# Kernel optimization log

Hardware: AMD Instinct MI355X
Metric: run time of the kernel (lower is better)

The kernel has to match this reference:

```python
import jax, jax.numpy as jnp
import numpy as np

B = 16384
F_IN = 768
F_OUT = 512

def setup_inputs() -> dict:
    key = jax.random.key(0)
    k1, k2, k3, k4, k5, k6 = jax.random.split(key, 6)
    # densified sparse multi-hot boards (post to_dense())
    stm = jax.random.uniform(k1, (B, F_IN), dtype=jnp.float32)
    nstm = jax.random.uniform(k2, (B, F_IN), dtype=jnp.float32)
    s1 = 1.0 / np.sqrt(F_IN)
    s2 = 1.0 / np.sqrt(2 * F_OUT)
    W1 = jax.random.normal(k3, (F_OUT, F_IN), dtype=jnp.float32) * s1
    b1 = jax.random.normal(k4, (F_OUT,), dtype=jnp.float32) * s1
    W2 = jax.random.normal(k5, (1, 2 * F_OUT), dtype=jnp.float32) * s2
    b2 = jax.random.normal(k6, (1,), dtype=jnp.float32) * s2
    return {"stm": stm, "nstm": nstm, "W1": W1, "b1": b1, "W2": W2, "b2": b2}

def reference(stm, nstm, W1, b1, W2, b2):
    # shared feature transformer applied to both perspectives
    stm_p = stm @ W1.T + b1    # [B, F_OUT]
    nstm_p = nstm @ W1.T + b1  # [B, F_OUT]
    hidden = jnp.clip(jnp.concatenate((stm_p, nstm_p), axis=1), 0.0, 1.0)  # [B, 2*F_OUT]
    return jax.nn.sigmoid(hidden @ W2.T + b2)  # [B, 1]
```

## Files before the change

### kernel.cpp

```cpp
#include <hip/hip_runtime.h>
#include <hip/hip_bf16.h>

#define BATCH 16384
#define FIN   768
#define FOUT  512

#define BK 32
#define NT (FIN / BK)

typedef __attribute__((ext_vector_type(8))) short short8;
typedef __attribute__((ext_vector_type(4))) float floatx4;

__device__ __forceinline__ unsigned int cvt_pk_bf16(float a, float b) {
    unsigned int r;
    asm("v_cvt_pk_bf16_f32 %0, %1, %2" : "=v"(r) : "v"(a), "v"(b));
    return r;
}

__device__ __forceinline__ void load_lds_16(const void* g, void* l) {
    __builtin_amdgcn_global_load_lds(
        (const __attribute__((address_space(1))) unsigned int*)g,
        (__attribute__((address_space(3))) unsigned int*)l,
        16, 0, 0);
}

__global__ __launch_bounds__(256) void cvt_w1(
    const float* __restrict__ W1, unsigned short* __restrict__ W1b)
{
    int base = (blockIdx.x * 256 + threadIdx.x) * 8;
    float4 a = *(const float4*)(W1 + base);
    float4 b = *(const float4*)(W1 + base + 4);
    uint4 o;
    o.x = cvt_pk_bf16(a.x, a.y); o.y = cvt_pk_bf16(a.z, a.w);
    o.z = cvt_pk_bf16(b.x, b.y); o.w = cvt_pk_bf16(b.z, b.w);
    *(uint4*)(W1b + base) = o;
}

__global__ __launch_bounds__(1024, 4) void pn_gemm(
    const float* __restrict__ stm, const float* __restrict__ nstm,
    const unsigned short* __restrict__ W1b, const float* __restrict__ b1,
    const float* __restrict__ W2, const float* __restrict__ b2,
    float* __restrict__ out)
{
    __shared__ __align__(16) unsigned short As[2][128 * 32];
    __shared__ __align__(16) unsigned short Bs[2][512 * 32];

    const int tid  = threadIdx.x;
    const int lane = tid & 63;
    const int wave = tid >> 6;
    const int wrow = wave >> 3;
    const int wcol = wave & 7;
    const int quad = lane >> 4;
    const int l16  = lane & 15;
    const int l3   = l16 & 3;

    const int b0 = blockIdx.x * 64;

    const int arow = tid >> 2;
    const int ach  = tid & 3;
    const float* aSrc = nullptr;
    if (wave < 8)
        aSrc = ((arow < 64) ? stm  + (size_t)(b0 + arow) * FIN
                            : nstm + (size_t)(b0 + arow - 64) * FIN) + ach * 8;
    const int aOff = arow * 32 + (ach ^ (arow & 3)) * 8;

    const int brow = lane >> 2;
    const int bch  = (lane & 3) ^ (brow & 3);

    floatx4 acc[4][4];
    #pragma unroll
    for (int i = 0; i < 4; ++i)
        #pragma unroll
        for (int j = 0; j < 4; ++j)
            acc[i][j] = (floatx4)0.0f;

    float4 ap0, ap1;
    if (wave < 8) {
        ap0 = *(const float4*)(aSrc);
        ap1 = *(const float4*)(aSrc + 4);
    }
    #pragma unroll
    for (int i = 0; i < 2; ++i) {
        const int J = wave * 2 + i;
        load_lds_16(W1b + (size_t)(J * 16 + brow) * FIN + bch * 8,
                    &Bs[0][J * 16 * 32]);
    }

    for (int t = 0; t < NT; ++t) {
        const int cur = t & 1;
        const int nxt = cur ^ 1;

        if (wave < 8) {
            uint4 o;
            o.x = cvt_pk_bf16(ap0.x, ap0.y); o.y = cvt_pk_bf16(ap0.z, ap0.w);
            o.z = cvt_pk_bf16(ap1.x, ap1.y); o.w = cvt_pk_bf16(ap1.z, ap1.w);
            *(uint4*)(&As[cur][aOff]) = o;
        }
        __syncthreads();

        if (t + 1 < NT) {
            const int kn = (t + 1) * BK;
            #pragma unroll
            for (int i = 0; i < 2; ++i) {
                const int J = wave * 2 + i;
                load_lds_16(W1b + (size_t)(J * 16 + brow) * FIN + kn + bch * 8,
                            &Bs[nxt][J * 16 * 32]);
            }
            if (wave < 8) {
                ap0 = *(const float4*)(aSrc + kn);
                ap1 = *(const float4*)(aSrc + kn + 4);
            }
        }

        short8 af[4], bfr[4];
        #pragma unroll
        for (int mi = 0; mi < 4; ++mi) {
            const int m = wrow * 64 + mi * 16 + l16;
            af[mi] = *(const short8*)(&As[cur][m * 32 + ((quad ^ l3) * 8)]);
        }
        #pragma unroll
        for (int ni = 0; ni < 4; ++ni) {
            const int n = wcol * 64 + ni * 16 + l16;
            bfr[ni] = *(const short8*)(&Bs[cur][n * 32 + ((quad ^ l3) * 8)]);
        }
        #pragma unroll
        for (int mi = 0; mi < 4; ++mi)
            #pragma unroll
            for (int ni = 0; ni < 4; ++ni)
                acc[mi][ni] = __builtin_amdgcn_mfma_f32_16x16x32_bf16(
                    af[mi], bfr[ni], acc[mi][ni], 0, 0, 0);
    }

    float b1v[4], w2v[4];
    #pragma unroll
    for (int ni = 0; ni < 4; ++ni) {
        int col = wcol * 64 + ni * 16 + l16;
        b1v[ni] = b1[col];
        w2v[ni] = W2[wrow * FOUT + col];
    }

    __syncthreads();
    float* Epi = (float*)As;

    #pragma unroll
    for (int mi = 0; mi < 4; ++mi) {
        #pragma unroll
        for (int r = 0; r < 4; ++r) {
            float s = 0.0f;
            #pragma unroll
            for (int ni = 0; ni < 4; ++ni) {
                float h = acc[mi][ni][r] + b1v[ni];
                h = fminf(fmaxf(h, 0.0f), 1.0f);
                s += h * w2v[ni];
            }
            s += __shfl_xor(s, 1);
            s += __shfl_xor(s, 2);
            s += __shfl_xor(s, 4);
            s += __shfl_xor(s, 8);
            if (l16 == 0) {
                Epi[(wrow * 64 + mi * 16 + quad * 4 + r) * 8 + wcol] = s;
            }
        }
    }
    __syncthreads();

    if (tid < 64) {
        float x = b2[0];
        #pragma unroll
        for (int j = 0; j < 8; ++j)
            x += Epi[tid * 8 + j] + Epi[(tid + 64) * 8 + j];
        out[b0 + tid] = 1.0f / (1.0f + expf(-x));
    }
}

extern "C" void kernel_launch(void* const* d_in, const int* in_sizes, int n_in,
                              void* d_out, int out_size, void* d_ws, size_t ws_size,
                              hipStream_t stream)
{
    (void)in_sizes; (void)n_in; (void)out_size; (void)ws_size;
    const float* stm  = (const float*)d_in[0];
    const float* nstm = (const float*)d_in[1];
    const float* W1   = (const float*)d_in[2];
    const float* b1   = (const float*)d_in[3];
    const float* W2   = (const float*)d_in[4];
    const float* b2   = (const float*)d_in[5];
    float* out = (float*)d_out;
    unsigned short* W1b = (unsigned short*)d_ws;

    cvt_w1<<<dim3((FOUT * FIN) / (256 * 8)), dim3(256), 0, stream>>>(W1, W1b);
    pn_gemm<<<dim3(BATCH / 64), dim3(1024), 0, stream>>>(
        stm, nstm, W1b, b1, W2, b2, out);
}
```

Baseline: 147.7 us.

## Retile GEMM to 128-row by 256-column blocks with split-N partial sums

Changes each block from covering 64 batch rows (128 A rows) by all 512 outputs to 128 batch rows (256 A rows) by half of the outputs. All 16 waves now load A, instead of half of them sitting idle during A staging. Partial dot products for each N half are written to a workspace, and a new finish kernel adds them with b2 and applies the sigmoid. The A tile per block grows, so each B byte is reused across more rows. In exchange, the fp32 A inputs are read twice, once per N half, and there is an extra kernel launch and a round trip through global memory for the partial sums.

```diff
diff --git a/kernel.cpp b/kernel.cpp
--- a/kernel.cpp
+++ b/kernel.cpp
@@ -7,6 +7,8 @@
 
 #define BK 32
 #define NT (FIN / BK)
+#define BM 128
+#define BN 256
 
 typedef __attribute__((ext_vector_type(8))) short short8;
 typedef __attribute__((ext_vector_type(4))) float floatx4;
@@ -39,33 +41,36 @@
 __global__ __launch_bounds__(1024, 4) void pn_gemm(
     const float* __restrict__ stm, const float* __restrict__ nstm,
     const unsigned short* __restrict__ W1b, const float* __restrict__ b1,
-    const float* __restrict__ W2, const float* __restrict__ b2,
-    float* __restrict__ out)
+    const float* __restrict__ W2, float* __restrict__ P)
 {
-    __shared__ __align__(16) unsigned short As[2][128 * 32];
-    __shared__ __align__(16) unsigned short Bs[2][512 * 32];
+    __shared__ __align__(16) unsigned short As[2][256 * 32];
+    __shared__ __align__(16) unsigned short Bs[2][256 * 32];
 
     const int tid  = threadIdx.x;
     const int lane = tid & 63;
     const int wave = tid >> 6;
-    const int wrow = wave >> 3;
-    const int wcol = wave & 7;
+    const int wr   = wave >> 2;
+    const int wc   = wave & 3;
     const int quad = lane >> 4;
     const int l16  = lane & 15;
     const int l3   = l16 & 3;
 
-    const int b0 = blockIdx.x * 64;
+    const int bm    = blockIdx.x >> 1;
+    const int n_idx = blockIdx.x & 1;
+    const int b0    = bm * BM;
+    const int n0    = n_idx * BN;
 
     const int arow = tid >> 2;
     const int ach  = tid & 3;
-    const float* aSrc = nullptr;
-    if (wave < 8)
-        aSrc = ((arow < 64) ? stm  + (size_t)(b0 + arow) * FIN
-                            : nstm + (size_t)(b0 + arow - 64) * FIN) + ach * 8;
+    const float* aSrc =
+        ((arow < BM) ? stm  + (size_t)(b0 + arow) * FIN
+                     : nstm + (size_t)(b0 + arow - BM) * FIN) + ach * 8;
     const int aOff = arow * 32 + (ach ^ (arow & 3)) * 8;
 
     const int brow = lane >> 2;
     const int bch  = (lane & 3) ^ (brow & 3);
+    const unsigned short* bSrc =
+        W1b + (size_t)(n0 + wave * 16 + brow) * FIN + bch * 8;
 
     floatx4 acc[4][4];
     #pragma unroll
@@ -74,23 +79,15 @@
         for (int j = 0; j < 4; ++j)
             acc[i][j] = (floatx4)0.0f;
 
-    float4 ap0, ap1;
-    if (wave < 8) {
-        ap0 = *(const float4*)(aSrc);
-        ap1 = *(const float4*)(aSrc + 4);
-    }
-    #pragma unroll
-    for (int i = 0; i < 2; ++i) {
-        const int J = wave * 2 + i;
-        load_lds_16(W1b + (size_t)(J * 16 + brow) * FIN + bch * 8,
-                    &Bs[0][J * 16 * 32]);
-    }
+    float4 ap0 = *(const float4*)(aSrc);
+    float4 ap1 = *(const float4*)(aSrc + 4);
+    load_lds_16(bSrc, &Bs[0][wave * 512]);
 
     for (int t = 0; t < NT; ++t) {
         const int cur = t & 1;
         const int nxt = cur ^ 1;
 
-        if (wave < 8) {
+        {
             uint4 o;
             o.x = cvt_pk_bf16(ap0.x, ap0.y); o.y = cvt_pk_bf16(ap0.z, ap0.w);
             o.z = cvt_pk_bf16(ap1.x, ap1.y); o.w = cvt_pk_bf16(ap1.z, ap1.w);
@@ -100,27 +97,20 @@
 
         if (t + 1 < NT) {
             const int kn = (t + 1) * BK;
-            #pragma unroll
-            for (int i = 0; i < 2; ++i) {
-                const int J = wave * 2 + i;
-                load_lds_16(W1b + (size_t)(J * 16 + brow) * FIN + kn + bch * 8,
-                            &Bs[nxt][J * 16 * 32]);
-            }
-            if (wave < 8) {
-                ap0 = *(const float4*)(aSrc + kn);
-                ap1 = *(const float4*)(aSrc + kn + 4);
-            }
+            load_lds_16(bSrc + kn, &Bs[nxt][wave * 512]);
+            ap0 = *(const float4*)(aSrc + kn);
+            ap1 = *(const float4*)(aSrc + kn + 4);
         }
 
         short8 af[4], bfr[4];
         #pragma unroll
         for (int mi = 0; mi < 4; ++mi) {
-            const int m = wrow * 64 + mi * 16 + l16;
+            const int m = wr * 64 + mi * 16 + l16;
             af[mi] = *(const short8*)(&As[cur][m * 32 + ((quad ^ l3) * 8)]);
         }
         #pragma unroll
         for (int ni = 0; ni < 4; ++ni) {
-            const int n = wcol * 64 + ni * 16 + l16;
+            const int n = wc * 64 + ni * 16 + l16;
             bfr[ni] = *(const short8*)(&Bs[cur][n * 32 + ((quad ^ l3) * 8)]);
         }
         #pragma unroll
@@ -132,11 +122,12 @@
     }
 
     float b1v[4], w2v[4];
+    const float* w2base = (wr < 2) ? W2 : W2 + FOUT;
     #pragma unroll
     for (int ni = 0; ni < 4; ++ni) {
-        int col = wcol * 64 + ni * 16 + l16;
+        int col = n0 + wc * 64 + ni * 16 + l16;
         b1v[ni] = b1[col];
-        w2v[ni] = W2[wrow * FOUT + col];
+        w2v[ni] = w2base[col];
     }
 
     __syncthreads();
@@ -158,19 +149,28 @@
             s += __shfl_xor(s, 4);
             s += __shfl_xor(s, 8);
             if (l16 == 0) {
-                Epi[(wrow * 64 + mi * 16 + quad * 4 + r) * 8 + wcol] = s;
+                Epi[(wr * 64 + mi * 16 + quad * 4 + r) * 4 + wc] = s;
             }
         }
     }
     __syncthreads();
 
-    if (tid < 64) {
-        float x = b2[0];
+    if (tid < BM) {
+        float x = 0.0f;
         #pragma unroll
-        for (int j = 0; j < 8; ++j)
-            x += Epi[tid * 8 + j] + Epi[(tid + 64) * 8 + j];
-        out[b0 + tid] = 1.0f / (1.0f + expf(-x));
+        for (int j = 0; j < 4; ++j)
+            x += Epi[tid * 4 + j] + Epi[(tid + BM) * 4 + j];
+        P[n_idx * BATCH + b0 + tid] = x;
     }
+}
+
+__global__ __launch_bounds__(256) void finish(
+    const float* __restrict__ P, const float* __restrict__ b2,
+    float* __restrict__ out)
+{
+    int i = blockIdx.x * 256 + threadIdx.x;
+    float x = b2[0] + P[i] + P[BATCH + i];
+    out[i] = 1.0f / (1.0f + expf(-x));
 }
 
 extern "C" void kernel_launch(void* const* d_in, const int* in_sizes, int n_in,
@@ -186,8 +186,10 @@
     const float* b2   = (const float*)d_in[5];
     float* out = (float*)d_out;
     unsigned short* W1b = (unsigned short*)d_ws;
+    float* P = (float*)((char*)d_ws + FOUT * FIN * 2);
 
     cvt_w1<<<dim3((FOUT * FIN) / (256 * 8)), dim3(256), 0, stream>>>(W1, W1b);
-    pn_gemm<<<dim3(BATCH / 64), dim3(1024), 0, stream>>>(
-        stm, nstm, W1b, b1, W2, b2, out);
+    pn_gemm<<<dim3((BATCH / BM) * 2), dim3(1024), 0, stream>>>(
+        stm, nstm, W1b, b1, W2, P);
+    finish<<<dim3(BATCH / 256), dim3(256), 0, stream>>>(P, b2, out);
 }
```

After: 154.3 us. +4.5%, slower.
